# Optimization experiments

Measured on AMD Instinct MI355X. Metric: run time of the kernel, lower is better.

The kernel has to match this reference:

```python
import jax, jax.numpy as jnp
import numpy as np

B, L, D, H, E = 64, 128, 768, 2, 131072  # graphs, nodes/graph, hidden, heads, edges
N = B * L
C = D // H  # per-head channels


def _transformer_conv(x, src, dst, wq, bq, wk, bk, wv, bv, ws, bs):
    # PyG TransformerConv (concat=True, root_weight=True, beta=False)
    n = x.shape[0]
    q = (x @ wq + bq).reshape(n, H, C)
    k = (x @ wk + bk).reshape(n, H, C)
    v = (x @ wv + bv).reshape(n, H, C)
    # per-edge attention logits [E, H]
    logits = jnp.sum(q[dst] * k[src], axis=-1) * (1.0 / np.sqrt(C))
    # scatter softmax over incoming edges of each dst node
    m = jax.ops.segment_max(logits, dst, num_segments=n)
    e = jnp.exp(logits - m[dst])
    s = jax.ops.segment_sum(e, dst, num_segments=n)
    alpha = e / s[dst]  # [E, H]
    msg = alpha[..., None] * v[src]  # [E, H, C]
    agg = jax.ops.segment_sum(msg, dst, num_segments=n).reshape(n, D)
    return agg + x @ ws + bs


def setup_inputs() -> dict:
    key = jax.random.key(0)
    ks = jax.random.split(key, 24)
    x = jax.random.normal(ks[0], (N, D), jnp.float32)
    # within-graph random edges
    dst = jax.random.randint(ks[1], (E,), 0, N)
    off = jax.random.randint(ks[2], (E,), 0, L)
    src = (dst // L) * L + off
    edge_index = jnp.stack([src, dst]).astype(jnp.int32)

    def lin(k, i, o):
        return jax.random.normal(k, (i, o), jnp.float32) * 0.02

    inp = {"x": x, "edge_index": edge_index}
    i = 3
    for layer in ("1", "2"):
        for nm in ("wq", "wk", "wv", "ws"):
            inp[nm + layer] = lin(ks[i], D, D); i += 1
            inp["b" + nm[1] + layer] = jnp.zeros((D,), jnp.float32)
    inp["atti_w"] = lin(ks[i], 2 * D, D); i += 1
    inp["atti_b"] = jnp.zeros((D,), jnp.float32)
    inp["atts_w"] = lin(ks[i], D, 1); i += 1
    inp["atts_b"] = jnp.zeros((1,), jnp.float32)
    inp["fc1_w"] = lin(ks[i], D, D); i += 1
    inp["fc1_b"] = jnp.zeros((D,), jnp.float32)
    inp["fc2_w"] = lin(ks[i], D, 3); i += 1
    inp["fc2_b"] = jnp.zeros((3,), jnp.float32)
    return inp


def reference(x, edge_index, wq1, bq1, wk1, bk1, wv1, bv1, ws1, bs1,
              wq2, bq2, wk2, bk2, wv2, bv2, ws2, bs2,
              atti_w, atti_b, atts_w, atts_b, fc1_w, fc1_b, fc2_w, fc2_b):
    src, dst = edge_index[0], edge_index[1]
    h = jax.nn.relu(_transformer_conv(x, src, dst, wq1, bq1, wk1, bk1, wv1, bv1, ws1, bs1))
    h = jax.nn.relu(_transformer_conv(h, src, dst, wq2, bq2, wk2, bk2, wv2, bv2, ws2, bs2))
    # pad(): equal-size graphs -> reshape, mask all-valid (x_mask all False)
    hp = h.reshape(B, L, D)
    # attention pooling (eval path): query = first node of each graph
    x_q = jnp.broadcast_to(hp[:, :1], hp.shape)  # [B, L, D]
    x_c = jax.nn.relu(jnp.concatenate([x_q, hp], axis=-1) @ atti_w + atti_b)
    score = x_c @ atts_w + atts_b  # [B, L, 1]
    score = jax.nn.softmax(score, axis=1)
    pooled = jnp.sum(hp * score, axis=1)  # [B, D]
    out = jnp.tanh(pooled @ fc1_w + fc1_b) @ fc2_w + fc2_b
    return jax.nn.log_softmax(out, axis=-1)
```

## Files before the change

kernel.cpp:

```cpp
#include <hip/hip_runtime.h>

#define NN 8192
#define DD 768
#define EE 131072
#define BBg 64
#define LLn 128
#define CCh 384

typedef unsigned short u16;
typedef unsigned char u8;
typedef __attribute__((ext_vector_type(8))) short short8;
typedef __attribute__((ext_vector_type(4))) float f32x4;

__device__ __forceinline__ float b2f(u16 u) {
    union { unsigned int i; float f; } x; x.i = ((unsigned int)u) << 16; return x.f;
}
__device__ __forceinline__ u16 f2b(float f) {
    union { float f; unsigned int i; } x; x.f = f;
    unsigned int r = x.i + 0x7fffu + ((x.i >> 16) & 1u);
    return (u16)(r >> 16);
}
__device__ __forceinline__ void gload16(const void* g, void* l) {
    __builtin_amdgcn_global_load_lds((const __attribute__((address_space(1))) void*)g,
                                     (__attribute__((address_space(3))) void*)l, 16, 0, 0);
}

__global__ void cnt_build(const int* __restrict__ srcp, const int* __restrict__ dstp,
                          unsigned int* __restrict__ cnt32) {
    int e = blockIdx.x * 256 + threadIdx.x;
    int d = dstp[e], s = srcp[e];
    int g = d >> 7;
    int idx = (g << 14) + ((d & 127) << 7) + (s & 127);
    atomicAdd(&cnt32[idx >> 2], 1u << ((idx & 3) * 8));
}

__global__ void f32_to_bf16_vec(const float* __restrict__ in, u16* __restrict__ out, int n4) {
    int i = blockIdx.x * 256 + threadIdx.x;
    if (i >= n4) return;
    float4 v = ((const float4*)in)[i];
    ushort4 o; o.x = f2b(v.x); o.y = f2b(v.y); o.z = f2b(v.z); o.w = f2b(v.w);
    ((ushort4*)out)[i] = o;
}

struct TP { const float* src; u16* dst; int rowOff; };
struct TP11 { TP a[11]; };

__global__ __launch_bounds__(256) void transpose_batched(TP11 args) {
    __shared__ float tile[64][65];
    TP tp = args.a[blockIdx.z];
    int n0 = blockIdx.x * 64, k0 = blockIdx.y * 64;
    int t = threadIdx.x;
    int tc = t & 63, tr = t >> 6;
#pragma unroll
    for (int i = 0; i < 16; i++)
        tile[tr + i * 4][tc] = tp.src[(size_t)(tp.rowOff + k0 + tr + i * 4) * DD + n0 + tc];
    __syncthreads();
#pragma unroll
    for (int i = 0; i < 16; i++) {
        int row = tr + i * 4;
        tp.dst[(size_t)(n0 + row) * DD + k0 + tc] = f2b(tile[tc][row]);
    }
}

enum { EPI_F32 = 1, EPI_TANH = 3 };

__global__ __launch_bounds__(256) void gemm_bf16(const u16* __restrict__ A,
                                                 const u16* __restrict__ Wt,
                                                 const float* __restrict__ bias,
                                                 void* __restrict__ outp, int K, int mode) {
    __shared__ u16 As[64][72];
    __shared__ u16 Bs[64][72];
    const int m0 = blockIdx.y * 64, n0 = blockIdx.x * 64;
    const int t = threadIdx.x;
    const int lane = t & 63, w = t >> 6;
    const int tr = t >> 2, tc = (t & 3) * 16;
    f32x4 acc[4] = {{0,0,0,0},{0,0,0,0},{0,0,0,0},{0,0,0,0}};
    const int fRow = lane & 15;
    const int fK = (lane >> 4) * 8;

    for (int k0 = 0; k0 < K; k0 += 64) {
        int4 a0 = *(const int4*)(A + (size_t)(m0 + tr) * K + k0 + tc);
        int4 a1 = *(const int4*)(A + (size_t)(m0 + tr) * K + k0 + tc + 8);
        int4 b0 = *(const int4*)(Wt + (size_t)(n0 + tr) * K + k0 + tc);
        int4 b1 = *(const int4*)(Wt + (size_t)(n0 + tr) * K + k0 + tc + 8);
        __syncthreads();
        *(int4*)&As[tr][tc] = a0; *(int4*)&As[tr][tc + 8] = a1;
        *(int4*)&Bs[tr][tc] = b0; *(int4*)&Bs[tr][tc + 8] = b1;
        __syncthreads();
#pragma unroll
        for (int s = 0; s < 2; s++) {
            short8 af = *(const short8*)&As[w * 16 + fRow][s * 32 + fK];
#pragma unroll
            for (int g = 0; g < 4; g++) {
                short8 bf = *(const short8*)&Bs[g * 16 + fRow][s * 32 + fK];
                acc[g] = __builtin_amdgcn_mfma_f32_16x16x32_bf16(af, bf, acc[g], 0, 0, 0);
            }
        }
    }
    const int colLocal = lane & 15;
    const int rowLocal = (lane >> 4) * 4;
#pragma unroll
    for (int g = 0; g < 4; g++) {
        int col = n0 + g * 16 + colLocal;
        float bv = bias ? bias[col] : 0.f;
#pragma unroll
        for (int i = 0; i < 4; i++) {
            int row = m0 + w * 16 + rowLocal + i;
            float v = acc[g][i] + bv;
            if (mode == EPI_TANH) v = tanhf(v);
            ((float*)outp)[(size_t)row * DD + col] = v;
        }
    }
}

__global__ __launch_bounds__(256, 2) void gemm256(const u16* __restrict__ A,
                                                  const u16* __restrict__ Wt,
                                                  const float* __restrict__ b0,
                                                  const float* __restrict__ b1,
                                                  const float* __restrict__ b2,
                                                  const float* __restrict__ b3,
                                                  u16* __restrict__ o0, u16* __restrict__ o1,
                                                  u16* __restrict__ o2, u16* __restrict__ o3) {
    __shared__ u16 As[256 * 64];
    __shared__ u16 Bs[128 * 64];
    const int K = DD;
    const int t = threadIdx.x;
    const int lane = t & 63, w = t >> 6;
    const int wr = w >> 1, wc = w & 1;
    const int m0 = blockIdx.y * 256, n0 = blockIdx.x * 128;
    const int fRow = lane & 15, fThr = lane >> 4;
    f32x4 acc[8][4] = {};
    const u16* Abase = A + (size_t)m0 * K;
    const u16* Bbase = Wt + (size_t)n0 * K;

    for (int k0 = 0; k0 < K; k0 += 64) {
        __syncthreads();
#pragma unroll
        for (int i = 0; i < 8; i++) {
            int c = t + 256 * i;
            int row = c >> 3;
            int col = ((c & 7) ^ (row & 7)) * 8;
            gload16(Abase + (size_t)row * K + k0 + col, (char*)As + (size_t)c * 16);
        }
#pragma unroll
        for (int i = 0; i < 4; i++) {
            int c = t + 256 * i;
            int row = c >> 3;
            int col = ((c & 7) ^ (row & 7)) * 8;
            gload16(Bbase + (size_t)row * K + k0 + col, (char*)Bs + (size_t)c * 16);
        }
        __syncthreads();
#pragma unroll
        for (int kk = 0; kk < 64; kk += 32) {
            const int cjW = (kk >> 3) + fThr;
            short8 af[8], bf[4];
#pragma unroll
            for (int i = 0; i < 8; i++) {
                int R = wr * 128 + i * 16 + fRow;
                af[i] = *(const short8*)&As[(R * 8 + (cjW ^ (R & 7))) * 8];
            }
#pragma unroll
            for (int g = 0; g < 4; g++) {
                int R = wc * 64 + g * 16 + fRow;
                bf[g] = *(const short8*)&Bs[(R * 8 + (cjW ^ (R & 7))) * 8];
            }
#pragma unroll
            for (int i = 0; i < 8; i++)
#pragma unroll
                for (int g = 0; g < 4; g++)
                    acc[i][g] = __builtin_amdgcn_mfma_f32_16x16x32_bf16(af[i], bf[g], acc[i][g], 0, 0, 0);
        }
    }
    const int chunk = (n0 + wc * 64) / DD;
    const float* bp = (chunk == 0) ? b0 : (chunk == 1) ? b1 : (chunk == 2) ? b2 : b3;
    u16* op = (chunk == 0) ? o0 : (chunk == 1) ? o1 : (chunk == 2) ? o2 : o3;
    const int cb = n0 + wc * 64 - chunk * DD;
    if (chunk == 2) {
#pragma unroll
        for (int g = 0; g < 4; g++) {
            int col = cb + g * 16 + fRow;
            float bv = bp[col];
#pragma unroll
            for (int i = 0; i < 8; i++) {
                int rowb = m0 + wr * 128 + i * 16 + fThr * 4;
                ushort4 st;
                st.x = f2b(acc[i][g][0] + bv);
                st.y = f2b(acc[i][g][1] + bv);
                st.z = f2b(acc[i][g][2] + bv);
                st.w = f2b(acc[i][g][3] + bv);
                *(ushort4*)(op + (size_t)col * NN + rowb) = st;
            }
        }
    } else {
#pragma unroll
        for (int g = 0; g < 4; g++) {
            int col = cb + g * 16 + fRow;
            float bv = bp[col];
#pragma unroll
            for (int i = 0; i < 8; i++) {
                int rowb = m0 + wr * 128 + i * 16 + fThr * 4;
#pragma unroll
                for (int rr = 0; rr < 4; rr++)
                    op[(size_t)(rowb + rr) * DD + col] = f2b(acc[i][g][rr] + bv);
            }
        }
    }
}

__global__ __launch_bounds__(256) void gemm_xc(const u16* __restrict__ A,
                                               const u16* __restrict__ Wt,
                                               const u16* __restrict__ wt8,
                                               const float* __restrict__ atti_b,
                                               const float* __restrict__ atts_w,
                                               float* __restrict__ score) {
    __shared__ u16 As[128 * 64];
    __shared__ u16 Bs[128 * 64];
    __shared__ float aq_p[2][128];
    const int K = DD;
    const int t = threadIdx.x;
    const int lane = t & 63, w = t >> 6;
    const int wr = w >> 1, wc = w & 1;
    const int n0 = blockIdx.x * 128, m0 = blockIdx.y * 128;
    const int fRow = lane & 15, fThr = lane >> 4;

    {
        int col = t & 127, kh = t >> 7;
        const u16* xr = A + (size_t)m0 * DD + kh * 384;
        const u16* wr8 = wt8 + (size_t)(n0 + col) * DD + kh * 384;
        float s = 0.f;
#pragma unroll 8
        for (int j = 0; j < 96; j++) {
            ushort4 a4 = *(const ushort4*)(xr + j * 4);
            ushort4 b4 = *(const ushort4*)(wr8 + j * 4);
            s += b2f(a4.x) * b2f(b4.x) + b2f(a4.y) * b2f(b4.y)
               + b2f(a4.z) * b2f(b4.z) + b2f(a4.w) * b2f(b4.w);
        }
        aq_p[kh][col] = s;
    }

    f32x4 acc[4][4] = {};
    const u16* Abase = A + (size_t)m0 * K;
    const u16* Bbase = Wt + (size_t)n0 * K;
    for (int k0 = 0; k0 < K; k0 += 64) {
        __syncthreads();
#pragma unroll
        for (int i = 0; i < 4; i++) {
            int c = t + 256 * i;
            int row = c >> 3;
            int col = ((c & 7) ^ (row & 7)) * 8;
            gload16(Abase + (size_t)row * K + k0 + col, (char*)As + (size_t)c * 16);
            gload16(Bbase + (size_t)row * K + k0 + col, (char*)Bs + (size_t)c * 16);
        }
        __syncthreads();
#pragma unroll
        for (int kk = 0; kk < 64; kk += 32) {
            const int cjW = (kk >> 3) + fThr;
            short8 af[4], bf[4];
#pragma unroll
            for (int i = 0; i < 4; i++) {
                int R = wr * 64 + i * 16 + fRow;
                af[i] = *(const short8*)&As[(R * 8 + (cjW ^ (R & 7))) * 8];
            }
#pragma unroll
            for (int g = 0; g < 4; g++) {
                int R = wc * 64 + g * 16 + fRow;
                bf[g] = *(const short8*)&Bs[(R * 8 + (cjW ^ (R & 7))) * 8];
            }
#pragma unroll
            for (int i = 0; i < 4; i++)
#pragma unroll
                for (int g = 0; g < 4; g++)
                    acc[i][g] = __builtin_amdgcn_mfma_f32_16x16x32_bf16(af[i], bf[g], acc[i][g], 0, 0, 0);
        }
    }
    float rsum[4][4] = {};
#pragma unroll
    for (int g = 0; g < 4; g++) {
        int cl = wc * 64 + g * 16 + fRow;
        int col = n0 + cl;
        float bv = atti_b[col] + aq_p[0][cl] + aq_p[1][cl];
        float av = atts_w[col];
#pragma unroll
        for (int i = 0; i < 4; i++)
#pragma unroll
            for (int rr = 0; rr < 4; rr++) {
                float v = fmaxf(acc[i][g][rr] + bv, 0.f);
                rsum[i][rr] += v * av;
            }
    }
#pragma unroll
    for (int i = 0; i < 4; i++)
#pragma unroll
        for (int rr = 0; rr < 4; rr++) {
            float s = rsum[i][rr];
            s += __shfl_xor(s, 1, 16); s += __shfl_xor(s, 2, 16);
            s += __shfl_xor(s, 4, 16); s += __shfl_xor(s, 8, 16);
            if (fRow == 0)
                atomicAdd(&score[m0 + wr * 64 + i * 16 + fThr * 4 + rr], s);
        }
}

__global__ __launch_bounds__(256) void attn_fused(const u16* __restrict__ qb,
                                                  const u16* __restrict__ kb,
                                                  const u16* __restrict__ vT,
                                                  const u8* __restrict__ cnt,
                                                  const u16* __restrict__ hs,
                                                  u16* __restrict__ out) {
    __shared__ u16 As[64][72];
    __shared__ u16 Bs[128][72];
    __shared__ u16 Pl[64][136];
    __shared__ u16 Vt[64][136];
    const int half = blockIdx.x, hd = blockIdx.y, g = blockIdx.z;
    const int t = threadIdx.x;
    const int lane = t & 63, w = t >> 6;
    const int fRow = lane & 15, fThr = lane >> 4;
    const int dstBase = g * 128 + half * 64;
    const u16* Qb = qb + (size_t)dstBase * DD + hd * CCh;
    const u16* Kb = kb + (size_t)(g * 128) * DD + hd * CCh;

    f32x4 acc[8] = {};
    const int trA = t >> 2, tcA = (t & 3) * 16;
    const int trB = t >> 1, tcB = (t & 1) * 32;
    for (int k0 = 0; k0 < CCh; k0 += 64) {
        int4 a0 = *(const int4*)(Qb + (size_t)trA * DD + k0 + tcA);
        int4 a1 = *(const int4*)(Qb + (size_t)trA * DD + k0 + tcA + 8);
        int4 b0 = *(const int4*)(Kb + (size_t)trB * DD + k0 + tcB);
        int4 b1 = *(const int4*)(Kb + (size_t)trB * DD + k0 + tcB + 8);
        int4 b2 = *(const int4*)(Kb + (size_t)trB * DD + k0 + tcB + 16);
        int4 b3 = *(const int4*)(Kb + (size_t)trB * DD + k0 + tcB + 24);
        __syncthreads();
        *(int4*)&As[trA][tcA] = a0; *(int4*)&As[trA][tcA + 8] = a1;
        *(int4*)&Bs[trB][tcB] = b0; *(int4*)&Bs[trB][tcB + 8] = b1;
        *(int4*)&Bs[trB][tcB + 16] = b2; *(int4*)&Bs[trB][tcB + 24] = b3;
        __syncthreads();
#pragma unroll
        for (int kk = 0; kk < 64; kk += 32) {
            short8 af = *(const short8*)&As[w * 16 + fRow][kk + fThr * 8];
#pragma unroll
            for (int j = 0; j < 8; j++) {
                short8 bf = *(const short8*)&Bs[j * 16 + fRow][kk + fThr * 8];
                acc[j] = __builtin_amdgcn_mfma_f32_16x16x32_bf16(af, bf, acc[j], 0, 0, 0);
            }
        }
    }

    const float scale = 0.05103103630798288f;
    const u8* cg = cnt + ((size_t)g << 14);
    const int rbase = half * 64 + w * 16 + fThr * 4;
    float pv[8][4];
#pragma unroll
    for (int i = 0; i < 4; i++) {
        float m = -3.4e38f;
#pragma unroll
        for (int j = 0; j < 8; j++) {
            float c = (float)cg[(rbase + i) * 128 + j * 16 + fRow];
            float s = acc[j][i] * scale;
            pv[j][i] = c;
            if (c > 0.f) m = fmaxf(m, s);
        }
#pragma unroll
        for (int msk = 1; msk <= 8; msk <<= 1) m = fmaxf(m, __shfl_xor(m, msk, 16));
        float sum = 0.f;
#pragma unroll
        for (int j = 0; j < 8; j++) {
            float p = (pv[j][i] > 0.f) ? pv[j][i] * __expf(acc[j][i] * scale - m) : 0.f;
            pv[j][i] = p; sum += p;
        }
#pragma unroll
        for (int msk = 1; msk <= 8; msk <<= 1) sum += __shfl_xor(sum, msk, 16);
        float inv = (sum > 0.f) ? 1.f / sum : 0.f;
#pragma unroll
        for (int j = 0; j < 8; j++)
            Pl[w * 16 + fThr * 4 + i][j * 16 + fRow] = f2b(pv[j][i] * inv);
    }

    for (int cc = 0; cc < 6; cc++) {
        __syncthreads();
#pragma unroll
        for (int ii = 0; ii < 4; ii++) {
            int q = t + 256 * ii;
            int row = q >> 4, col = (q & 15) * 8;
            *(int4*)&Vt[row][col] =
                *(const int4*)(vT + (size_t)(hd * CCh + cc * 64 + row) * NN + g * 128 + col);
        }
        __syncthreads();
        f32x4 acc2[4] = {};
#pragma unroll
        for (int kk = 0; kk < 128; kk += 32) {
            short8 af = *(const short8*)&Pl[w * 16 + fRow][kk + fThr * 8];
#pragma unroll
            for (int j = 0; j < 4; j++) {
                short8 bf = *(const short8*)&Vt[j * 16 + fRow][kk + fThr * 8];
                acc2[j] = __builtin_amdgcn_mfma_f32_16x16x32_bf16(af, bf, acc2[j], 0, 0, 0);
            }
        }
#pragma unroll
        for (int j = 0; j < 4; j++) {
            int c = hd * CCh + cc * 64 + j * 16 + fRow;
#pragma unroll
            for (int i = 0; i < 4; i++) {
                int row = dstBase + w * 16 + fThr * 4 + i;
                size_t idx = (size_t)row * DD + c;
                float r = fmaxf(acc2[j][i] + b2f(hs[idx]), 0.f);
                out[idx] = f2b(r);
            }
        }
    }
}

__global__ __launch_bounds__(192) void pool_kernel(const float* __restrict__ score,
                                                   const u16* __restrict__ hx,
                                                   u16* __restrict__ pb) {
    int b = blockIdx.x, t = threadIdx.x;
    __shared__ float sprob[LLn];
    if (t < 64) {
        float s0 = score[b * LLn + t];
        float s1 = score[b * LLn + 64 + t];
        float mx = fmaxf(s0, s1);
#pragma unroll
        for (int m = 1; m <= 32; m <<= 1) mx = fmaxf(mx, __shfl_xor(mx, m, 64));
        float e0 = __expf(s0 - mx), e1 = __expf(s1 - mx);
        float sum = e0 + e1;
#pragma unroll
        for (int m = 1; m <= 32; m <<= 1) sum += __shfl_xor(sum, m, 64);
        float inv = 1.f / sum;
        sprob[t] = e0 * inv; sprob[t + 64] = e1 * inv;
    }
    __syncthreads();
    int c = t * 4;
    float a0 = 0, a1 = 0, a2 = 0, a3 = 0;
    for (int l = 0; l < LLn; l++) {
        float wl = sprob[l];
        ushort4 hv = *(const ushort4*)(hx + (size_t)(b * LLn + l) * DD + c);
        a0 += wl * b2f(hv.x); a1 += wl * b2f(hv.y); a2 += wl * b2f(hv.z); a3 += wl * b2f(hv.w);
    }
    ushort4 o; o.x = f2b(a0); o.y = f2b(a1); o.z = f2b(a2); o.w = f2b(a3);
    *(ushort4*)(pb + (size_t)b * DD + c) = o;
}

__global__ __launch_bounds__(256) void head2_kernel(const float* __restrict__ u,
                                                    const float* __restrict__ fc2w,
                                                    const float* __restrict__ fc2b,
                                                    float* __restrict__ outp) {
    int b = blockIdx.x, t = threadIdx.x;
    __shared__ float sred[4][3];
    float p0 = 0, p1 = 0, p2 = 0;
    for (int k = t; k < DD; k += 256) {
        float uv = u[(size_t)b * DD + k];
        p0 += uv * fc2w[k * 3 + 0]; p1 += uv * fc2w[k * 3 + 1]; p2 += uv * fc2w[k * 3 + 2];
    }
#pragma unroll
    for (int m = 1; m <= 32; m <<= 1) {
        p0 += __shfl_xor(p0, m, 64); p1 += __shfl_xor(p1, m, 64); p2 += __shfl_xor(p2, m, 64);
    }
    int w = t >> 6, lane = t & 63;
    if (lane == 0) { sred[w][0] = p0; sred[w][1] = p1; sred[w][2] = p2; }
    __syncthreads();
    if (t == 0) {
        float z0 = fc2b[0], z1 = fc2b[1], z2 = fc2b[2];
        for (int i = 0; i < 4; i++) { z0 += sred[i][0]; z1 += sred[i][1]; z2 += sred[i][2]; }
        float mx = fmaxf(z0, fmaxf(z1, z2));
        float lse = mx + logf(__expf(z0 - mx) + __expf(z1 - mx) + __expf(z2 - mx));
        outp[b * 3 + 0] = z0 - lse; outp[b * 3 + 1] = z1 - lse; outp[b * 3 + 2] = z2 - lse;
    }
}

static inline char* carve(char*& p, size_t bytes) {
    char* r = p;
    p += (bytes + 255) & ~(size_t)255;
    return r;
}

extern "C" void kernel_launch(void* const* d_in, const int* in_sizes, int n_in,
                              void* d_out, int out_size, void* d_ws, size_t ws_size,
                              hipStream_t stream) {
    const float* x = (const float*)d_in[0];
    const int* ei = (const int*)d_in[1];
    const int* srcp = ei;
    const int* dstp = ei + EE;
    const float* wL[8] = {(const float*)d_in[2], (const float*)d_in[4], (const float*)d_in[6],
                          (const float*)d_in[8], (const float*)d_in[10], (const float*)d_in[12],
                          (const float*)d_in[14], (const float*)d_in[16]};
    const float* bL[8] = {(const float*)d_in[3], (const float*)d_in[5], (const float*)d_in[7],
                          (const float*)d_in[9], (const float*)d_in[11], (const float*)d_in[13],
                          (const float*)d_in[15], (const float*)d_in[17]};
    const float* atti_w = (const float*)d_in[18];
    const float* atti_b = (const float*)d_in[19];
    const float* atts_w = (const float*)d_in[20];
    const float* fc1_w = (const float*)d_in[22];
    const float* fc1_b = (const float*)d_in[23];
    const float* fc2_w = (const float*)d_in[24];
    const float* fc2_b = (const float*)d_in[25];
    float* outp = (float*)d_out;

    char* p = (char*)d_ws;
    const size_t ndb = (size_t)NN * DD * 2;
    const size_t wsz = (size_t)DD * DD * 2;
    u16* qb = (u16*)carve(p, ndb);
    u16* kb = (u16*)carve(p, ndb);
    u16* vt = (u16*)carve(p, ndb);
    u16* xb = (u16*)carve(p, ndb);
    u16* hb = (u16*)carve(p, ndb);
    u16* hs = (u16*)carve(p, ndb);
    u16* wtcat1 = (u16*)carve(p, wsz * 4);
    u16* wtcat2 = (u16*)carve(p, wsz * 4);
    u16* wt8 = (u16*)carve(p, wsz);
    u16* wt9 = (u16*)carve(p, wsz);
    u16* wtfc1 = (u16*)carve(p, wsz);
    u16* pb = (u16*)carve(p, (size_t)BBg * DD * 2);
    float* uu = (float*)carve(p, (size_t)BBg * DD * 4);
    u8* cnt = (u8*)carve(p, (size_t)BBg * 128 * 128);
    float* score = (float*)carve(p, NN * 4);

    hipMemsetAsync(cnt, 0, (size_t)BBg * 128 * 128, stream);
    hipMemsetAsync(score, 0, NN * 4, stream);
    cnt_build<<<EE / 256, 256, 0, stream>>>(srcp, dstp, (unsigned int*)cnt);

    f32_to_bf16_vec<<<(NN * DD / 4) / 256, 256, 0, stream>>>(x, xb, NN * DD / 4);
    TP11 tps;
    for (int i = 0; i < 4; i++) tps.a[i] = {wL[i], wtcat1 + (size_t)i * DD * DD, 0};
    for (int i = 0; i < 4; i++) tps.a[4 + i] = {wL[4 + i], wtcat2 + (size_t)i * DD * DD, 0};
    tps.a[8] = {atti_w, wt8, 0};
    tps.a[9] = {atti_w, wt9, DD};
    tps.a[10] = {fc1_w, wtfc1, 0};
    transpose_batched<<<dim3(12, 12, 11), 256, 0, stream>>>(tps);

    dim3 gf(24, 32);
    dim3 ga(2, 2, BBg);
    gemm256<<<gf, 256, 0, stream>>>(xb, wtcat1, bL[0], bL[1], bL[2], bL[3], qb, kb, vt, hs);
    attn_fused<<<ga, 256, 0, stream>>>(qb, kb, vt, cnt, hs, hb);
    gemm256<<<gf, 256, 0, stream>>>(hb, wtcat2, bL[4], bL[5], bL[6], bL[7], qb, kb, vt, hs);
    attn_fused<<<ga, 256, 0, stream>>>(qb, kb, vt, cnt, hs, xb);

    gemm_xc<<<dim3(6, 64), 256, 0, stream>>>(xb, wt9, wt8, atti_b, atts_w, score);
    pool_kernel<<<BBg, 192, 0, stream>>>(score, xb, pb);

    gemm_bf16<<<dim3(12, 1), 256, 0, stream>>>(pb, wtfc1, fc1_b, uu, DD, EPI_TANH);
    head2_kernel<<<BBg, 256, 0, stream>>>(uu, fc2_w, fc2_b, outp);
}
```

Baseline: 352.3 us.

## Split fused attention into QK-softmax and PV kernels for more parallelism

The fused attention kernel, launched on only 256 blocks that each looped over six V column chunks, is split into two kernels. attn_qk computes the masked softmax probabilities and writes them to a global P buffer. attn_pv then runs on 768 blocks, one per V column chunk, and each block computes 128 rows. The goal is to fill more of the GPU's compute units and drop the serial chunk loop. The cost is an extra kernel launch per layer and a round trip of P through global memory.

```diff
diff --git a/kernel.cpp b/kernel.cpp
--- a/kernel.cpp
+++ b/kernel.cpp
@@ -300,16 +300,13 @@
         }
 }
 
-__global__ __launch_bounds__(256) void attn_fused(const u16* __restrict__ qb,
-                                                  const u16* __restrict__ kb,
-                                                  const u16* __restrict__ vT,
-                                                  const u8* __restrict__ cnt,
-                                                  const u16* __restrict__ hs,
-                                                  u16* __restrict__ out) {
+__global__ __launch_bounds__(256) void attn_qk(const u16* __restrict__ qb,
+                                               const u16* __restrict__ kb,
+                                               const u8* __restrict__ cnt,
+                                               u16* __restrict__ P) {
     __shared__ u16 As[64][72];
     __shared__ u16 Bs[128][72];
     __shared__ u16 Pl[64][136];
-    __shared__ u16 Vt[64][136];
     const int half = blockIdx.x, hd = blockIdx.y, g = blockIdx.z;
     const int t = threadIdx.x;
     const int lane = t & 63, w = t >> 6;
@@ -373,35 +370,65 @@
         for (int j = 0; j < 8; j++)
             Pl[w * 16 + fThr * 4 + i][j * 16 + fRow] = f2b(pv[j][i] * inv);
     }
-
-    for (int cc = 0; cc < 6; cc++) {
-        __syncthreads();
-#pragma unroll
-        for (int ii = 0; ii < 4; ii++) {
-            int q = t + 256 * ii;
-            int row = q >> 4, col = (q & 15) * 8;
-            *(int4*)&Vt[row][col] =
-                *(const int4*)(vT + (size_t)(hd * CCh + cc * 64 + row) * NN + g * 128 + col);
-        }
-        __syncthreads();
-        f32x4 acc2[4] = {};
-#pragma unroll
-        for (int kk = 0; kk < 128; kk += 32) {
-            short8 af = *(const short8*)&Pl[w * 16 + fRow][kk + fThr * 8];
-#pragma unroll
-            for (int j = 0; j < 4; j++) {
-                short8 bf = *(const short8*)&Vt[j * 16 + fRow][kk + fThr * 8];
-                acc2[j] = __builtin_amdgcn_mfma_f32_16x16x32_bf16(af, bf, acc2[j], 0, 0, 0);
-            }
-        }
-#pragma unroll
-        for (int j = 0; j < 4; j++) {
-            int c = hd * CCh + cc * 64 + j * 16 + fRow;
-#pragma unroll
-            for (int i = 0; i < 4; i++) {
-                int row = dstBase + w * 16 + fThr * 4 + i;
-                size_t idx = (size_t)row * DD + c;
-                float r = fmaxf(acc2[j][i] + b2f(hs[idx]), 0.f);
+    __syncthreads();
+    u16* Pbase = P + ((size_t)(g * 2 + hd) * 128 + half * 64) * 128;
+#pragma unroll
+    for (int ii = 0; ii < 4; ii++) {
+        int c = t + 256 * ii;
+        int row = c >> 4, ch = c & 15;
+        *(short8*)(Pbase + (size_t)row * 128 + ch * 8) = *(const short8*)&Pl[row][ch * 8];
+    }
+}
+
+__global__ __launch_bounds__(256) void attn_pv(const u16* __restrict__ P,
+                                               const u16* __restrict__ vT,
+                                               const u16* __restrict__ hs,
+                                               u16* __restrict__ out) {
+    __shared__ u16 Vt[64][136];
+    const int cc = blockIdx.x, hd = blockIdx.y, g = blockIdx.z;
+    const int t = threadIdx.x;
+    const int lane = t & 63, w = t >> 6;
+    const int fRow = lane & 15, fThr = lane >> 4;
+    const u16* Pbase = P + (size_t)(g * 2 + hd) * 128 * 128;
+
+#pragma unroll
+    for (int ii = 0; ii < 4; ii++) {
+        int q = t + 256 * ii;
+        int row = q >> 4, col = (q & 15) * 8;
+        *(int4*)&Vt[row][col] =
+            *(const int4*)(vT + (size_t)(hd * CCh + cc * 64 + row) * NN + g * 128 + col);
+    }
+    __syncthreads();
+
+    f32x4 acc[2][4] = {};
+#pragma unroll
+    for (int kk = 0; kk < 128; kk += 32) {
+        short8 af[2], bf[4];
+#pragma unroll
+        for (int i = 0; i < 2; i++) {
+            int row = w * 32 + i * 16 + fRow;
+            af[i] = *(const short8*)(Pbase + (size_t)row * 128 + kk + fThr * 8);
+        }
+#pragma unroll
+        for (int j = 0; j < 4; j++)
+            bf[j] = *(const short8*)&Vt[j * 16 + fRow][kk + fThr * 8];
+#pragma unroll
+        for (int i = 0; i < 2; i++)
+#pragma unroll
+            for (int j = 0; j < 4; j++)
+                acc[i][j] = __builtin_amdgcn_mfma_f32_16x16x32_bf16(af[i], bf[j], acc[i][j], 0, 0, 0);
+    }
+#pragma unroll
+    for (int j = 0; j < 4; j++) {
+        int col = hd * CCh + cc * 64 + j * 16 + fRow;
+#pragma unroll
+        for (int i = 0; i < 2; i++) {
+            int rowb = w * 32 + i * 16 + fThr * 4;
+#pragma unroll
+            for (int rr = 0; rr < 4; rr++) {
+                int row = g * 128 + rowb + rr;
+                size_t idx = (size_t)row * DD + col;
+                float r = fmaxf(acc[i][j][rr] + b2f(hs[idx]), 0.f);
                 out[idx] = f2b(r);
             }
         }
@@ -502,6 +529,7 @@
     u16* xb = (u16*)carve(p, ndb);
     u16* hb = (u16*)carve(p, ndb);
     u16* hs = (u16*)carve(p, ndb);
+    u16* Pbuf = (u16*)carve(p, (size_t)BBg * 2 * 128 * 128 * 2);
     u16* wtcat1 = (u16*)carve(p, wsz * 4);
     u16* wtcat2 = (u16*)carve(p, wsz * 4);
     u16* wt8 = (u16*)carve(p, wsz);
@@ -526,11 +554,14 @@
     transpose_batched<<<dim3(12, 12, 11), 256, 0, stream>>>(tps);
 
     dim3 gf(24, 32);
-    dim3 ga(2, 2, BBg);
+    dim3 gq(2, 2, BBg);
+    dim3 gp(6, 2, BBg);
     gemm256<<<gf, 256, 0, stream>>>(xb, wtcat1, bL[0], bL[1], bL[2], bL[3], qb, kb, vt, hs);
-    attn_fused<<<ga, 256, 0, stream>>>(qb, kb, vt, cnt, hs, hb);
+    attn_qk<<<gq, 256, 0, stream>>>(qb, kb, cnt, Pbuf);
+    attn_pv<<<gp, 256, 0, stream>>>(Pbuf, vt, hs, hb);
     gemm256<<<gf, 256, 0, stream>>>(hb, wtcat2, bL[4], bL[5], bL[6], bL[7], qb, kb, vt, hs);
-    attn_fused<<<ga, 256, 0, stream>>>(qb, kb, vt, cnt, hs, xb);
+    attn_qk<<<gq, 256, 0, stream>>>(qb, kb, cnt, Pbuf);
+    attn_pv<<<gp, 256, 0, stream>>>(Pbuf, vt, hs, xb);
 
     gemm_xc<<<dim3(6, 64), 256, 0, stream>>>(xb, wt9, wt8, atti_b, atts_w, score);
     pool_kernel<<<BBg, 192, 0, stream>>>(score, xb, pb);
```

New measurement: 367.2 us. 4.2% more time.

## Fuse prep kernels, memsets, and pooling/fc1/fc2 tail into fewer launches

Applied to the files above, without the earlier changes.

Merges the memsets and bf16 conversion into one prep kernel, folds edge count building into the batched weight transpose launch as an extra z-slice, and fuses attention pooling, fc1+tanh and fc2+log_softmax into one per-graph kernel. The aim is to cut kernel launch overhead and intermediate global buffers. The fused fc1 now uses scalar dot products per block, with each graph's block re-reading the full fc1 weight and uncoalesced per-thread row reads, instead of MFMA. That could slow the tail.

```diff
diff --git a/kernel.cpp b/kernel.cpp
--- a/kernel.cpp
+++ b/kernel.cpp
@@ -25,30 +25,38 @@
                                      (__attribute__((address_space(3))) void*)l, 16, 0, 0);
 }
 
-__global__ void cnt_build(const int* __restrict__ srcp, const int* __restrict__ dstp,
-                          unsigned int* __restrict__ cnt32) {
-    int e = blockIdx.x * 256 + threadIdx.x;
-    int d = dstp[e], s = srcp[e];
-    int g = d >> 7;
-    int idx = (g << 14) + ((d & 127) << 7) + (s & 127);
-    atomicAdd(&cnt32[idx >> 2], 1u << ((idx & 3) * 8));
-}
-
-__global__ void f32_to_bf16_vec(const float* __restrict__ in, u16* __restrict__ out, int n4) {
+__global__ __launch_bounds__(256) void prep_kernel(const float* __restrict__ in,
+                                                   u16* __restrict__ out,
+                                                   unsigned int* __restrict__ cnt32,
+                                                   float* __restrict__ score) {
     int i = blockIdx.x * 256 + threadIdx.x;
-    if (i >= n4) return;
     float4 v = ((const float4*)in)[i];
     ushort4 o; o.x = f2b(v.x); o.y = f2b(v.y); o.z = f2b(v.z); o.w = f2b(v.w);
     ((ushort4*)out)[i] = o;
+    if (blockIdx.x < 1024) cnt32[i] = 0;
+    else if (blockIdx.x < 1056) score[i - 1024 * 256] = 0.f;
 }
 
 struct TP { const float* src; u16* dst; int rowOff; };
 struct TP11 { TP a[11]; };
 
-__global__ __launch_bounds__(256) void transpose_batched(TP11 args) {
+__global__ __launch_bounds__(256) void combo_kernel(TP11 args,
+                                                    const int* __restrict__ srcp,
+                                                    const int* __restrict__ dstp,
+                                                    unsigned int* __restrict__ cnt32) {
     __shared__ float tile[64][65];
+    if (blockIdx.z == 11) {
+        for (int e = blockIdx.x * 256 + threadIdx.x; e < EE; e += 144 * 256) {
+            int d = dstp[e], s = srcp[e];
+            int g = d >> 7;
+            int idx = (g << 14) + ((d & 127) << 7) + (s & 127);
+            atomicAdd(&cnt32[idx >> 2], 1u << ((idx & 3) * 8));
+        }
+        return;
+    }
     TP tp = args.a[blockIdx.z];
-    int n0 = blockIdx.x * 64, k0 = blockIdx.y * 64;
+    int bx = blockIdx.x % 12, by = blockIdx.x / 12;
+    int n0 = bx * 64, k0 = by * 64;
     int t = threadIdx.x;
     int tc = t & 63, tr = t >> 6;
 #pragma unroll
@@ -59,57 +67,6 @@
     for (int i = 0; i < 16; i++) {
         int row = tr + i * 4;
         tp.dst[(size_t)(n0 + row) * DD + k0 + tc] = f2b(tile[tc][row]);
-    }
-}
-
-enum { EPI_F32 = 1, EPI_TANH = 3 };
-
-__global__ __launch_bounds__(256) void gemm_bf16(const u16* __restrict__ A,
-                                                 const u16* __restrict__ Wt,
-                                                 const float* __restrict__ bias,
-                                                 void* __restrict__ outp, int K, int mode) {
-    __shared__ u16 As[64][72];
-    __shared__ u16 Bs[64][72];
-    const int m0 = blockIdx.y * 64, n0 = blockIdx.x * 64;
-    const int t = threadIdx.x;
-    const int lane = t & 63, w = t >> 6;
-    const int tr = t >> 2, tc = (t & 3) * 16;
-    f32x4 acc[4] = {{0,0,0,0},{0,0,0,0},{0,0,0,0},{0,0,0,0}};
-    const int fRow = lane & 15;
-    const int fK = (lane >> 4) * 8;
-
-    for (int k0 = 0; k0 < K; k0 += 64) {
-        int4 a0 = *(const int4*)(A + (size_t)(m0 + tr) * K + k0 + tc);
-        int4 a1 = *(const int4*)(A + (size_t)(m0 + tr) * K + k0 + tc + 8);
-        int4 b0 = *(const int4*)(Wt + (size_t)(n0 + tr) * K + k0 + tc);
-        int4 b1 = *(const int4*)(Wt + (size_t)(n0 + tr) * K + k0 + tc + 8);
-        __syncthreads();
-        *(int4*)&As[tr][tc] = a0; *(int4*)&As[tr][tc + 8] = a1;
-        *(int4*)&Bs[tr][tc] = b0; *(int4*)&Bs[tr][tc + 8] = b1;
-        __syncthreads();
-#pragma unroll
-        for (int s = 0; s < 2; s++) {
-            short8 af = *(const short8*)&As[w * 16 + fRow][s * 32 + fK];
-#pragma unroll
-            for (int g = 0; g < 4; g++) {
-                short8 bf = *(const short8*)&Bs[g * 16 + fRow][s * 32 + fK];
-                acc[g] = __builtin_amdgcn_mfma_f32_16x16x32_bf16(af, bf, acc[g], 0, 0, 0);
-            }
-        }
-    }
-    const int colLocal = lane & 15;
-    const int rowLocal = (lane >> 4) * 4;
-#pragma unroll
-    for (int g = 0; g < 4; g++) {
-        int col = n0 + g * 16 + colLocal;
-        float bv = bias ? bias[col] : 0.f;
-#pragma unroll
-        for (int i = 0; i < 4; i++) {
-            int row = m0 + w * 16 + rowLocal + i;
-            float v = acc[g][i] + bv;
-            if (mode == EPI_TANH) v = tanhf(v);
-            ((float*)outp)[(size_t)row * DD + col] = v;
-        }
     }
 }
 
@@ -408,11 +365,18 @@
     }
 }
 
-__global__ __launch_bounds__(192) void pool_kernel(const float* __restrict__ score,
+__global__ __launch_bounds__(256) void tail_kernel(const float* __restrict__ score,
                                                    const u16* __restrict__ hx,
-                                                   u16* __restrict__ pb) {
+                                                   const u16* __restrict__ wtfc1,
+                                                   const float* __restrict__ fc1b,
+                                                   const float* __restrict__ fc2w,
+                                                   const float* __restrict__ fc2b,
+                                                   float* __restrict__ outp) {
     int b = blockIdx.x, t = threadIdx.x;
     __shared__ float sprob[LLn];
+    __shared__ u16 psh[DD];
+    __shared__ float su[DD];
+    __shared__ float sred[4][3];
     if (t < 64) {
         float s0 = score[b * LLn + t];
         float s1 = score[b * LLn + 64 + t];
@@ -427,26 +391,36 @@
         sprob[t] = e0 * inv; sprob[t + 64] = e1 * inv;
     }
     __syncthreads();
-    int c = t * 4;
-    float a0 = 0, a1 = 0, a2 = 0, a3 = 0;
-    for (int l = 0; l < LLn; l++) {
-        float wl = sprob[l];
-        ushort4 hv = *(const ushort4*)(hx + (size_t)(b * LLn + l) * DD + c);
-        a0 += wl * b2f(hv.x); a1 += wl * b2f(hv.y); a2 += wl * b2f(hv.z); a3 += wl * b2f(hv.w);
-    }
-    ushort4 o; o.x = f2b(a0); o.y = f2b(a1); o.z = f2b(a2); o.w = f2b(a3);
-    *(ushort4*)(pb + (size_t)b * DD + c) = o;
-}
-
-__global__ __launch_bounds__(256) void head2_kernel(const float* __restrict__ u,
-                                                    const float* __restrict__ fc2w,
-                                                    const float* __restrict__ fc2b,
-                                                    float* __restrict__ outp) {
-    int b = blockIdx.x, t = threadIdx.x;
-    __shared__ float sred[4][3];
+    if (t < 192) {
+        int c = t * 4;
+        float a0 = 0, a1 = 0, a2 = 0, a3 = 0;
+        for (int l = 0; l < LLn; l++) {
+            float wl = sprob[l];
+            ushort4 hv = *(const ushort4*)(hx + (size_t)(b * LLn + l) * DD + c);
+            a0 += wl * b2f(hv.x); a1 += wl * b2f(hv.y); a2 += wl * b2f(hv.z); a3 += wl * b2f(hv.w);
+        }
+        ushort4 o; o.x = f2b(a0); o.y = f2b(a1); o.z = f2b(a2); o.w = f2b(a3);
+        *(ushort4*)(psh + c) = o;
+    }
+    __syncthreads();
+#pragma unroll
+    for (int jj = 0; jj < 3; jj++) {
+        int j = t + jj * 256;
+        float s = fc1b[j];
+        const u16* wrow = wtfc1 + (size_t)j * DD;
+#pragma unroll 8
+        for (int k = 0; k < DD; k += 4) {
+            ushort4 w4 = *(const ushort4*)(wrow + k);
+            ushort4 p4 = *(const ushort4*)(psh + k);
+            s += b2f(p4.x) * b2f(w4.x) + b2f(p4.y) * b2f(w4.y)
+               + b2f(p4.z) * b2f(w4.z) + b2f(p4.w) * b2f(w4.w);
+        }
+        su[j] = tanhf(s);
+    }
+    __syncthreads();
     float p0 = 0, p1 = 0, p2 = 0;
     for (int k = t; k < DD; k += 256) {
-        float uv = u[(size_t)b * DD + k];
+        float uv = su[k];
         p0 += uv * fc2w[k * 3 + 0]; p1 += uv * fc2w[k * 3 + 1]; p2 += uv * fc2w[k * 3 + 2];
     }
 #pragma unroll
@@ -507,23 +481,18 @@
     u16* wt8 = (u16*)carve(p, wsz);
     u16* wt9 = (u16*)carve(p, wsz);
     u16* wtfc1 = (u16*)carve(p, wsz);
-    u16* pb = (u16*)carve(p, (size_t)BBg * DD * 2);
-    float* uu = (float*)carve(p, (size_t)BBg * DD * 4);
     u8* cnt = (u8*)carve(p, (size_t)BBg * 128 * 128);
     float* score = (float*)carve(p, NN * 4);
 
-    hipMemsetAsync(cnt, 0, (size_t)BBg * 128 * 128, stream);
-    hipMemsetAsync(score, 0, NN * 4, stream);
-    cnt_build<<<EE / 256, 256, 0, stream>>>(srcp, dstp, (unsigned int*)cnt);
-
-    f32_to_bf16_vec<<<(NN * DD / 4) / 256, 256, 0, stream>>>(x, xb, NN * DD / 4);
+    prep_kernel<<<6144, 256, 0, stream>>>(x, xb, (unsigned int*)cnt, score);
+
     TP11 tps;
     for (int i = 0; i < 4; i++) tps.a[i] = {wL[i], wtcat1 + (size_t)i * DD * DD, 0};
     for (int i = 0; i < 4; i++) tps.a[4 + i] = {wL[4 + i], wtcat2 + (size_t)i * DD * DD, 0};
     tps.a[8] = {atti_w, wt8, 0};
     tps.a[9] = {atti_w, wt9, DD};
     tps.a[10] = {fc1_w, wtfc1, 0};
-    transpose_batched<<<dim3(12, 12, 11), 256, 0, stream>>>(tps);
+    combo_kernel<<<dim3(144, 1, 12), 256, 0, stream>>>(tps, srcp, dstp, (unsigned int*)cnt);
 
     dim3 gf(24, 32);
     dim3 ga(2, 2, BBg);
@@ -533,8 +502,6 @@
     attn_fused<<<ga, 256, 0, stream>>>(qb, kb, vt, cnt, hs, xb);
 
     gemm_xc<<<dim3(6, 64), 256, 0, stream>>>(xb, wt9, wt8, atti_b, atts_w, score);
-    pool_kernel<<<BBg, 192, 0, stream>>>(score, xb, pb);
-
-    gemm_bf16<<<dim3(12, 1), 256, 0, stream>>>(pb, wtfc1, fc1_b, uu, DD, EPI_TANH);
-    head2_kernel<<<BBg, 256, 0, stream>>>(uu, fc2_w, fc2_b, outp);
-}
+
+    tail_kernel<<<BBg, 256, 0, stream>>>(score, xb, wtfc1, fc1_b, fc2_w, fc2_b, outp);
+}
```

Result: slower. 365.8 us (+3.8%).
